# Performance work log

Measured on AMD Instinct MI355X. Metric: run time of the kernel, lower is better.

## Reference

```python
import jax, jax.numpy as jnp
import numpy as np

EMBED_DIM = 1024
NUM_HEADS = 16
HEAD_DIM = EMBED_DIM // NUM_HEADS
ROPE_BASE = 10000.0


def setup_inputs() -> dict:
    key = jax.random.key(0)
    ks = jax.random.split(key, 5)
    B, S, E = 4, 2048, EMBED_DIM
    hidden = jax.random.normal(ks[0], (B, S, E), dtype=jnp.float32)
    sc_in = 1.0 / np.sqrt(E)
    qkv_w = jax.random.normal(ks[1], (3 * E, E), dtype=jnp.float32) * sc_in
    qkv_b = jnp.zeros((3 * E,), dtype=jnp.float32)
    proj_w = jax.random.normal(ks[2], (E, E), dtype=jnp.float32) * sc_in
    proj_b = jnp.zeros((E,), dtype=jnp.float32)
    return {"hidden": hidden, "qkv_w": qkv_w, "qkv_b": qkv_b,
            "proj_w": proj_w, "proj_b": proj_b}


def _rope_cos_sin(position_ids, head_dim, base):
    # position_ids: [B, S] int; returns cos/sin of shape [B, 1, S, head_dim]
    inv_freq = 1.0 / (base ** (jnp.arange(0, head_dim, 2, dtype=jnp.float32) / head_dim))
    freqs = position_ids.astype(jnp.float32)[..., None] * inv_freq  # [B,S,hd/2]
    emb = jnp.concatenate([freqs, freqs], axis=-1)                  # [B,S,hd]
    return jnp.cos(emb)[:, None], jnp.sin(emb)[:, None]


def _rotate_half(x):
    x1, x2 = jnp.split(x, 2, axis=-1)
    return jnp.concatenate([-x2, x1], axis=-1)


def reference(hidden, qkv_w, qkv_b, proj_w, proj_b):
    B, S, E = hidden.shape
    H, hd = NUM_HEADS, HEAD_DIM
    qkv = hidden @ qkv_w.T + qkv_b                    # [B,S,3E]
    qkv = qkv.reshape(B, S, 3, H, hd).transpose(2, 0, 3, 1, 4)  # [3,B,H,S,hd]
    q, k, v = qkv[0], qkv[1], qkv[2]
    pos = jnp.broadcast_to(jnp.arange(S)[None, :], (B, S))
    cos, sin = _rope_cos_sin(pos, hd, ROPE_BASE)      # [B,1,S,hd]
    q = q * cos + _rotate_half(q) * sin
    k = k * cos + _rotate_half(k) * sin
    scale = 1.0 / jnp.sqrt(jnp.float32(hd))
    scores = jnp.einsum("bhsd,bhtd->bhst", q, k) * scale
    attn = jax.nn.softmax(scores, axis=-1)
    out = jnp.einsum("bhst,bhtd->bhsd", attn, v)      # [B,H,S,hd]
    out = out.transpose(0, 2, 1, 3).reshape(B, S, E)
    return out @ proj_w.T + proj_b
```

## Files before the change

kernel.cpp:

```cpp
#include <hip/hip_runtime.h>
#include <cstdint>
#include <cstddef>

typedef _Float16 f16;
typedef __attribute__((ext_vector_type(4))) float f32x4;
typedef __attribute__((ext_vector_type(8))) _Float16 f16x8;
typedef __attribute__((ext_vector_type(4))) _Float16 f16x4;

#define S_SEQ 2048
#define E_DIM 1024

#define OFF_HID   0ull
#define OFF_QKVW  8388608ull
#define OFF_PROJW 11534336ull
#define OFF_Q     12582912ull
#define OFF_K     20971520ull
#define OFF_VT    29360128ull
#define OFF_AO    37748736ull

__device__ __forceinline__ void async_copy16(const void* g, void* l) {
  __builtin_amdgcn_global_load_lds(
      (const __attribute__((address_space(1))) unsigned int*)g,
      (__attribute__((address_space(3))) unsigned int*)l, 16, 0, 0);
}

__device__ __forceinline__ f16x8 lds_read_b128(const f16* p) {
  f16x8 r;
  const __attribute__((address_space(3))) f16* p3 =
      (const __attribute__((address_space(3))) f16*)p;
  asm volatile("ds_read_b128 %0, %1" : "=v"(r) : "v"(p3));
  return r;
}

__device__ __forceinline__ float fast_exp2(float x) {
#if __has_builtin(__builtin_amdgcn_exp2f)
  return __builtin_amdgcn_exp2f(x);
#else
  return __expf(x * 0.6931471805599453f);
#endif
}

__device__ __forceinline__ int2 xcd_swizzle() {
  int lin = blockIdx.y * gridDim.x + blockIdx.x;
  int by = ((lin & 7) << 3) | ((lin >> 3) & 7);
  int bx = lin >> 6;
  return make_int2(bx, by);
}

__global__ __launch_bounds__(256) void cvt_kernel(const float* __restrict__ hid,
                                                  const float* __restrict__ qw,
                                                  const float* __restrict__ pw,
                                                  f16* __restrict__ ws) {
  long i = (long)blockIdx.x * 256 + threadIdx.x;
  const float* src;
  f16* dst;
  long idx;
  if (i < 2097152L) { src = hid; dst = ws + OFF_HID;  idx = i; }
  else if (i < 2883584L) { src = qw; dst = ws + OFF_QKVW; idx = i - 2097152L; }
  else { src = pw; dst = ws + OFF_PROJW; idx = i - 2883584L; }
  float4 v = *(const float4*)(src + idx * 4);
  f16x4 o = { (f16)v.x, (f16)v.y, (f16)v.z, (f16)v.w };
  *(f16x4*)(dst + idx * 4) = o;
}

template <int MODE>
__global__ __launch_bounds__(256)
void gemm_kernel(const f16* __restrict__ A, const f16* __restrict__ Bm,
                 const float* __restrict__ bias,
                 f16* __restrict__ q_out, f16* __restrict__ k_out,
                 f16* __restrict__ vT_out, float* __restrict__ f_out) {
  __shared__ __align__(16) f16 As[2][2][128 * 32];
  __shared__ __align__(16) f16 Bs[2][2][128 * 32];
  const int tid = threadIdx.x;
  const int wave = tid >> 6;
  const int lane = tid & 63;
  const int q4 = lane >> 4;
  const int l16 = lane & 15;
  const int2 sw = xcd_swizzle();
  const int bxs = sw.x;
  const int m0 = sw.y * 128;
  const int n0 = bxs * 128;
  const int wr = (wave >> 1) * 64;
  const int wc = (wave & 1) * 64;
  f32x4 acc[4][4] = {};

  const int srow = tid >> 2;
  const int scol = (tid & 3) * 8;

  auto stage = [&](int kt, int kh, int b) {
    const f16* as = A + (size_t)(m0 + srow) * 1024 + kt * 64 + kh * 32 + scol;
    async_copy16(as,             &As[b][kh][wave * 512]);
    async_copy16(as + 64 * 1024, &As[b][kh][2048 + wave * 512]);
    const f16* bs = Bm + (size_t)(n0 + srow) * 1024 + kt * 64 + kh * 32 + scol;
    async_copy16(bs,             &Bs[b][kh][wave * 512]);
    async_copy16(bs + 64 * 1024, &Bs[b][kh][2048 + wave * 512]);
  };

#define PHASE(T, KH, DO_STAGE, VMN)                                          \
  {                                                                          \
    const int cb_ = (T) & 1;                                                 \
    f16x8 af[4], bf[4];                                                      \
    _Pragma("unroll")                                                        \
    for (int mt = 0; mt < 4; ++mt)                                           \
      af[mt] = lds_read_b128(&As[cb_][KH][(wr + mt * 16 + l16) * 32 + q4 * 8]); \
    _Pragma("unroll")                                                        \
    for (int nt = 0; nt < 4; ++nt)                                           \
      bf[nt] = lds_read_b128(&Bs[cb_][KH][(wc + nt * 16 + l16) * 32 + q4 * 8]); \
    if (DO_STAGE) stage((T) + 1, KH, cb_ ^ 1);                               \
    __builtin_amdgcn_s_barrier();                                            \
    asm volatile("s_waitcnt lgkmcnt(0)" ::: "memory");                       \
    __builtin_amdgcn_sched_barrier(0);                                       \
    __builtin_amdgcn_s_setprio(1);                                           \
    _Pragma("unroll")                                                        \
    for (int mt = 0; mt < 4; ++mt)                                           \
      _Pragma("unroll")                                                      \
      for (int nt = 0; nt < 4; ++nt)                                         \
        acc[mt][nt] = __builtin_amdgcn_mfma_f32_16x16x32_f16(                \
            af[mt], bf[nt], acc[mt][nt], 0, 0, 0);                           \
    __builtin_amdgcn_s_setprio(0);                                           \
    __builtin_amdgcn_sched_barrier(0);                                       \
    asm volatile("s_waitcnt vmcnt(" #VMN ")" ::: "memory");                  \
    __builtin_amdgcn_s_barrier();                                            \
  }

  stage(0, 0, 0);
  stage(0, 1, 0);
  asm volatile("s_waitcnt vmcnt(4)" ::: "memory");
  __builtin_amdgcn_s_barrier();

  for (int t = 0; t < 15; ++t) {
    PHASE(t, 0, 1, 4);
    PHASE(t, 1, 1, 4);
  }
  PHASE(15, 0, 0, 0);
  PHASE(15, 1, 0, 0);
#undef PHASE

  if constexpr (MODE == 0) {
    const int part = bxs >> 3;
    const int h = (((bxs & 7) * 128) + wc) >> 6;
    float bv[4];
    for (int nt = 0; nt < 4; ++nt) bv[nt] = bias[n0 + wc + nt * 16 + l16];
    if (part < 2) {
      f16* outp = (part == 0) ? q_out : k_out;
      const float qscale = (part == 0) ? 0.18033688011112042f : 1.0f;
      float invf[2];
      for (int nt = 0; nt < 2; ++nt)
        invf[nt] = __expf(-(float)(nt * 16 + l16) * 0.2878231366242557f);
      for (int mt = 0; mt < 4; ++mt) {
        int mbase = m0 + wr + mt * 16 + q4 * 4;
        for (int r = 0; r < 4; ++r) {
          int mm = mbase + r;
          int b = mm >> 11, s = mm & 2047;
          size_t rowb = ((size_t)((b * 16 + h) * 2048 + s)) * 64;
          for (int nt = 0; nt < 2; ++nt) {
            float x1 = acc[mt][nt][r] + bv[nt];
            float x2 = acc[mt][nt + 2][r] + bv[nt + 2];
            float ang = (float)s * invf[nt];
            float sn, cs;
            __sincosf(ang, &sn, &cs);
            float o1 = (x1 * cs - x2 * sn) * qscale;
            float o2 = (x2 * cs + x1 * sn) * qscale;
            int d1 = nt * 16 + l16;
            outp[rowb + d1] = (f16)o1;
            outp[rowb + d1 + 32] = (f16)o2;
          }
        }
      }
    } else {
      for (int mt = 0; mt < 4; ++mt) {
        int mbase = m0 + wr + mt * 16 + q4 * 4;
        int b = mbase >> 11, s0 = mbase & 2047;
        for (int nt = 0; nt < 4; ++nt) {
          int d = nt * 16 + l16;
          size_t basei = ((size_t)((b * 16 + h) * 64 + d)) * 2048 + s0;
          f16x4 pk;
          for (int r = 0; r < 4; ++r) pk[r] = (f16)(acc[mt][nt][r] + bv[nt]);
          *(f16x4*)&vT_out[basei] = pk;
        }
      }
    }
  } else {
    float bv[4];
    for (int nt = 0; nt < 4; ++nt) bv[nt] = bias[n0 + wc + nt * 16 + l16];
    for (int mt = 0; mt < 4; ++mt)
      for (int r = 0; r < 4; ++r) {
        int mm = m0 + wr + mt * 16 + q4 * 4 + r;
        for (int nt = 0; nt < 4; ++nt)
          f_out[(size_t)mm * 1024 + n0 + wc + nt * 16 + l16] = acc[mt][nt][r] + bv[nt];
      }
  }
}

__global__ __launch_bounds__(256, 2)
void attn_kernel(const f16* __restrict__ Qg, const f16* __restrict__ Kg,
                 const f16* __restrict__ VTg, f16* __restrict__ AOg) {
  __shared__ __align__(16) f16 smem[2][8704];
  const int tid = threadIdx.x;
  const int wave = tid >> 6, lane = tid & 63;
  const int q4 = lane >> 4, l16 = lane & 15;
  const int2 sw = xcd_swizzle();
  const int qt = sw.x, bh = sw.y;
  const f16* Qb = Qg + (size_t)bh * (S_SEQ * 64);
  const f16* Kb = Kg + (size_t)bh * (S_SEQ * 64);
  const f16* Vb = VTg + (size_t)bh * (64 * S_SEQ);
  const int ws0 = wave * 64;

  f16x8 qf[4][2];
#pragma unroll
  for (int sn = 0; sn < 4; ++sn)
#pragma unroll
    for (int kf = 0; kf < 2; ++kf)
      qf[sn][kf] = *(const f16x8*)(Qb + (size_t)(qt * 256 + ws0 + sn * 16 + l16) * 64
                                      + kf * 32 + q4 * 8);

  f32x4 o[4][4] = {};
  f32x4 lacc[4] = {};
  f16x8 ones;
#pragma unroll
  for (int j = 0; j < 8; ++j) ones[j] = (f16)1.0f;

  const int srow = tid >> 3;
  const int scol = (tid & 7) * 8;

  const int kcs = scol >> 5;
  const int hs8 = ((scol >> 4) & 1) * 8;
  const int q0s = (scol & 15) >> 2;
  const int slot0 = kcs * 4 + q0s;
  const int swzA = (((slot0) ^ (srow & 7)) << 4) + hs8;
  const int swzB = (((slot0 + 1) ^ (srow & 7)) << 4) + hs8;

  int4 k0r = *(const int4*)(Kb + (size_t)srow * 64 + scol);
  int4 k1r = *(const int4*)(Kb + (size_t)(32 + srow) * 64 + scol);
  f16x8 v0r = *(const f16x8*)(Vb + (size_t)srow * 2048 + scol);
  f16x8 v1r = *(const f16x8*)(Vb + (size_t)(32 + srow) * 2048 + scol);
  {
    f16* Kn = smem[0];
    char* Vn = (char*)(smem[0] + 4608);
    *(int4*)(Kn + srow * 72 + scol) = k0r;
    *(int4*)(Kn + (32 + srow) * 72 + scol) = k1r;
    f16x4 lo0 = {v0r[0], v0r[1], v0r[2], v0r[3]};
    f16x4 hi0 = {v0r[4], v0r[5], v0r[6], v0r[7]};
    f16x4 lo1 = {v1r[0], v1r[1], v1r[2], v1r[3]};
    f16x4 hi1 = {v1r[4], v1r[5], v1r[6], v1r[7]};
    *(f16x4*)(Vn + srow * 128 + swzA) = lo0;
    *(f16x4*)(Vn + srow * 128 + swzB) = hi0;
    *(f16x4*)(Vn + (32 + srow) * 128 + swzA) = lo1;
    *(f16x4*)(Vn + (32 + srow) * 128 + swzB) = hi1;
  }
  __syncthreads();

  int cur = 0;
  for (int tt = 0; tt < 32; ++tt) {
    const f16* Kc = smem[cur];
    const char* Vc = (const char*)(smem[cur] + 4608);

    if (tt + 1 < 32) {
      const int t0n = (tt + 1) * 64;
      k0r = *(const int4*)(Kb + (size_t)(t0n + srow) * 64 + scol);
      k1r = *(const int4*)(Kb + (size_t)(t0n + 32 + srow) * 64 + scol);
      v0r = *(const f16x8*)(Vb + (size_t)srow * 2048 + t0n + scol);
      v1r = *(const f16x8*)(Vb + (size_t)(32 + srow) * 2048 + t0n + scol);
    }

    f16x8 kf0[4], kf1[4];
#pragma unroll
    for (int tm = 0; tm < 4; ++tm) {
      kf0[tm] = *(const f16x8*)(Kc + (tm * 16 + l16) * 72 + q4 * 8);
      kf1[tm] = *(const f16x8*)(Kc + (tm * 16 + l16) * 72 + 32 + q4 * 8);
    }
    f16x8 vf[4][2];
#pragma unroll
    for (int dm = 0; dm < 4; ++dm)
#pragma unroll
      for (int kc = 0; kc < 2; ++kc)
        vf[dm][kc] = *(const f16x8*)(Vc + (dm * 16 + l16) * 128 +
                                     (((kc * 4 + q4) ^ (l16 & 7)) << 4));

#pragma unroll
    for (int sn = 0; sn < 4; ++sn) {
      f32x4 st[4];
      __builtin_amdgcn_s_setprio(1);
#pragma unroll
      for (int tm = 0; tm < 4; ++tm) {
        f32x4 c = {0.f, 0.f, 0.f, 0.f};
        c = __builtin_amdgcn_mfma_f32_16x16x32_f16(kf0[tm], qf[sn][0], c, 0, 0, 0);
        c = __builtin_amdgcn_mfma_f32_16x16x32_f16(kf1[tm], qf[sn][1], c, 0, 0, 0);
        st[tm] = c;
      }
      __builtin_amdgcn_s_setprio(0);
#pragma unroll
      for (int tm = 0; tm < 4; ++tm)
#pragma unroll
        for (int r = 0; r < 4; ++r)
          st[tm][r] = fast_exp2(st[tm][r]);
#pragma unroll
      for (int kc = 0; kc < 2; ++kc) {
        f16x8 pf;
        pf[0] = (f16)st[kc * 2][0];
        pf[1] = (f16)st[kc * 2][1];
        pf[2] = (f16)st[kc * 2][2];
        pf[3] = (f16)st[kc * 2][3];
        pf[4] = (f16)st[kc * 2 + 1][0];
        pf[5] = (f16)st[kc * 2 + 1][1];
        pf[6] = (f16)st[kc * 2 + 1][2];
        pf[7] = (f16)st[kc * 2 + 1][3];
        __builtin_amdgcn_s_setprio(1);
        lacc[sn] = __builtin_amdgcn_mfma_f32_16x16x32_f16(ones, pf, lacc[sn], 0, 0, 0);
#pragma unroll
        for (int dm = 0; dm < 4; ++dm)
          o[dm][sn] = __builtin_amdgcn_mfma_f32_16x16x32_f16(vf[dm][kc], pf,
                                                             o[dm][sn], 0, 0, 0);
        __builtin_amdgcn_s_setprio(0);
      }
    }

    if (tt + 1 < 32) {
      f16* Kn = smem[cur ^ 1];
      char* Vn = (char*)(smem[cur ^ 1] + 4608);
      *(int4*)(Kn + srow * 72 + scol) = k0r;
      *(int4*)(Kn + (32 + srow) * 72 + scol) = k1r;
      f16x4 lo0 = {v0r[0], v0r[1], v0r[2], v0r[3]};
      f16x4 hi0 = {v0r[4], v0r[5], v0r[6], v0r[7]};
      f16x4 lo1 = {v1r[0], v1r[1], v1r[2], v1r[3]};
      f16x4 hi1 = {v1r[4], v1r[5], v1r[6], v1r[7]};
      *(f16x4*)(Vn + srow * 128 + swzA) = lo0;
      *(f16x4*)(Vn + srow * 128 + swzB) = hi0;
      *(f16x4*)(Vn + (32 + srow) * 128 + swzA) = lo1;
      *(f16x4*)(Vn + (32 + srow) * 128 + swzB) = hi1;
    }
    __syncthreads();
    cur ^= 1;
  }

  float inv_l[4];
#pragma unroll
  for (int sn = 0; sn < 4; ++sn) inv_l[sn] = 1.0f / lacc[sn][0];
  f16* Ot = smem[0];
#pragma unroll
  for (int sn = 0; sn < 4; ++sn) {
    int so = ws0 + sn * 16 + l16;
#pragma unroll
    for (int dm = 0; dm < 4; ++dm) {
      f16x4 w;
      w[0] = (f16)(o[dm][sn][0] * inv_l[sn]);
      w[1] = (f16)(o[dm][sn][1] * inv_l[sn]);
      w[2] = (f16)(o[dm][sn][2] * inv_l[sn]);
      w[3] = (f16)(o[dm][sn][3] * inv_l[sn]);
      *(f16x4*)(Ot + so * 64 + dm * 16 + q4 * 4) = w;
    }
  }
  __syncthreads();
  const int b = bh >> 4, h = bh & 15;
#pragma unroll
  for (int half = 0; half < 2; ++half) {
    const int sr = half * 128 + (tid >> 1), dh = (tid & 1) * 32;
    size_t gbase = ((size_t)(b * 2048 + qt * 256 + sr)) * 1024 + h * 64 + dh;
#pragma unroll
    for (int c = 0; c < 4; ++c) {
      f16x8 v = *(const f16x8*)(Ot + sr * 64 + dh + c * 8);
      *(f16x8*)(AOg + gbase + c * 8) = v;
    }
  }
}

extern "C" void kernel_launch(void* const* d_in, const int* in_sizes, int n_in,
                              void* d_out, int out_size, void* d_ws, size_t ws_size,
                              hipStream_t stream) {
  const float* hid   = (const float*)d_in[0];
  const float* qkvw  = (const float*)d_in[1];
  const float* qkvb  = (const float*)d_in[2];
  const float* projw = (const float*)d_in[3];
  const float* projb = (const float*)d_in[4];
  float* out = (float*)d_out;
  f16* ws = (f16*)d_ws;

  cvt_kernel<<<12288, 256, 0, stream>>>(hid, qkvw, projw, ws);
  gemm_kernel<0><<<dim3(24, 64), 256, 0, stream>>>(
      ws + OFF_HID, ws + OFF_QKVW, qkvb,
      ws + OFF_Q, ws + OFF_K, ws + OFF_VT, nullptr);
  attn_kernel<<<dim3(8, 64), 256, 0, stream>>>(
      ws + OFF_Q, ws + OFF_K, ws + OFF_VT, ws + OFF_AO);
  gemm_kernel<1><<<dim3(8, 64), 256, 0, stream>>>(
      ws + OFF_AO, ws + OFF_PROJW, projb,
      nullptr, nullptr, nullptr, out);
}
```

Measured before the change: 265.4 us.

## Load K and V fragments directly from global memory, dropping LDS staging

Removes the shared-memory double buffer for K and V tiles and has each wave load its MFMA fragments straight from global memory. K fragments are prefetched one tile ahead in registers, with two sets alternating. The setprio hints are dropped. This saves the LDS write/read traffic and the per-tile __syncthreads, but each of the four waves now fetches the same K/V data separately, relying on L1/L2 hits. V is read as 8-byte strided loads from the transposed layout, which are less coalesced.

New measurement: 362.0 us. 1.36x slower.

```diff
diff --git a/kernel.cpp b/kernel.cpp
--- a/kernel.cpp
+++ b/kernel.cpp
@@ -195,7 +195,7 @@
 __global__ __launch_bounds__(256, 2)
 void attn_kernel(const f16* __restrict__ Qg, const f16* __restrict__ Kg,
                  const f16* __restrict__ VTg, f16* __restrict__ AOg) {
-  __shared__ __align__(16) f16 smem[2][8704];
+  __shared__ __align__(16) f16 Ot[256 * 64];
   const int tid = threadIdx.x;
   const int wave = tid >> 6, lane = tid & 63;
   const int q4 = lane >> 4, l16 = lane & 15;
@@ -220,123 +220,88 @@
 #pragma unroll
   for (int j = 0; j < 8; ++j) ones[j] = (f16)1.0f;
 
-  const int srow = tid >> 3;
-  const int scol = (tid & 7) * 8;
-
-  const int kcs = scol >> 5;
-  const int hs8 = ((scol >> 4) & 1) * 8;
-  const int q0s = (scol & 15) >> 2;
-  const int slot0 = kcs * 4 + q0s;
-  const int swzA = (((slot0) ^ (srow & 7)) << 4) + hs8;
-  const int swzB = (((slot0 + 1) ^ (srow & 7)) << 4) + hs8;
-
-  int4 k0r = *(const int4*)(Kb + (size_t)srow * 64 + scol);
-  int4 k1r = *(const int4*)(Kb + (size_t)(32 + srow) * 64 + scol);
-  f16x8 v0r = *(const f16x8*)(Vb + (size_t)srow * 2048 + scol);
-  f16x8 v1r = *(const f16x8*)(Vb + (size_t)(32 + srow) * 2048 + scol);
-  {
-    f16* Kn = smem[0];
-    char* Vn = (char*)(smem[0] + 4608);
-    *(int4*)(Kn + srow * 72 + scol) = k0r;
-    *(int4*)(Kn + (32 + srow) * 72 + scol) = k1r;
-    f16x4 lo0 = {v0r[0], v0r[1], v0r[2], v0r[3]};
-    f16x4 hi0 = {v0r[4], v0r[5], v0r[6], v0r[7]};
-    f16x4 lo1 = {v1r[0], v1r[1], v1r[2], v1r[3]};
-    f16x4 hi1 = {v1r[4], v1r[5], v1r[6], v1r[7]};
-    *(f16x4*)(Vn + srow * 128 + swzA) = lo0;
-    *(f16x4*)(Vn + srow * 128 + swzB) = hi0;
-    *(f16x4*)(Vn + (32 + srow) * 128 + swzA) = lo1;
-    *(f16x4*)(Vn + (32 + srow) * 128 + swzB) = hi1;
-  }
-  __syncthreads();
-
-  int cur = 0;
-  for (int tt = 0; tt < 32; ++tt) {
-    const f16* Kc = smem[cur];
-    const char* Vc = (const char*)(smem[cur] + 4608);
-
-    if (tt + 1 < 32) {
-      const int t0n = (tt + 1) * 64;
-      k0r = *(const int4*)(Kb + (size_t)(t0n + srow) * 64 + scol);
-      k1r = *(const int4*)(Kb + (size_t)(t0n + 32 + srow) * 64 + scol);
-      v0r = *(const f16x8*)(Vb + (size_t)srow * 2048 + t0n + scol);
-      v1r = *(const f16x8*)(Vb + (size_t)(32 + srow) * 2048 + t0n + scol);
-    }
-
-    f16x8 kf0[4], kf1[4];
-#pragma unroll
-    for (int tm = 0; tm < 4; ++tm) {
-      kf0[tm] = *(const f16x8*)(Kc + (tm * 16 + l16) * 72 + q4 * 8);
-      kf1[tm] = *(const f16x8*)(Kc + (tm * 16 + l16) * 72 + 32 + q4 * 8);
-    }
-    f16x8 vf[4][2];
-#pragma unroll
-    for (int dm = 0; dm < 4; ++dm)
-#pragma unroll
-      for (int kc = 0; kc < 2; ++kc)
-        vf[dm][kc] = *(const f16x8*)(Vc + (dm * 16 + l16) * 128 +
-                                     (((kc * 4 + q4) ^ (l16 & 7)) << 4));
-
-#pragma unroll
-    for (int sn = 0; sn < 4; ++sn) {
-      f32x4 st[4];
-      __builtin_amdgcn_s_setprio(1);
-#pragma unroll
-      for (int tm = 0; tm < 4; ++tm) {
-        f32x4 c = {0.f, 0.f, 0.f, 0.f};
-        c = __builtin_amdgcn_mfma_f32_16x16x32_f16(kf0[tm], qf[sn][0], c, 0, 0, 0);
-        c = __builtin_amdgcn_mfma_f32_16x16x32_f16(kf1[tm], qf[sn][1], c, 0, 0, 0);
-        st[tm] = c;
-      }
-      __builtin_amdgcn_s_setprio(0);
-#pragma unroll
-      for (int tm = 0; tm < 4; ++tm)
-#pragma unroll
-        for (int r = 0; r < 4; ++r)
-          st[tm][r] = fast_exp2(st[tm][r]);
-#pragma unroll
-      for (int kc = 0; kc < 2; ++kc) {
-        f16x8 pf;
-        pf[0] = (f16)st[kc * 2][0];
-        pf[1] = (f16)st[kc * 2][1];
-        pf[2] = (f16)st[kc * 2][2];
-        pf[3] = (f16)st[kc * 2][3];
-        pf[4] = (f16)st[kc * 2 + 1][0];
-        pf[5] = (f16)st[kc * 2 + 1][1];
-        pf[6] = (f16)st[kc * 2 + 1][2];
-        pf[7] = (f16)st[kc * 2 + 1][3];
-        __builtin_amdgcn_s_setprio(1);
-        lacc[sn] = __builtin_amdgcn_mfma_f32_16x16x32_f16(ones, pf, lacc[sn], 0, 0, 0);
-#pragma unroll
-        for (int dm = 0; dm < 4; ++dm)
-          o[dm][sn] = __builtin_amdgcn_mfma_f32_16x16x32_f16(vf[dm][kc], pf,
-                                                             o[dm][sn], 0, 0, 0);
-        __builtin_amdgcn_s_setprio(0);
-      }
-    }
-
-    if (tt + 1 < 32) {
-      f16* Kn = smem[cur ^ 1];
-      char* Vn = (char*)(smem[cur ^ 1] + 4608);
-      *(int4*)(Kn + srow * 72 + scol) = k0r;
-      *(int4*)(Kn + (32 + srow) * 72 + scol) = k1r;
-      f16x4 lo0 = {v0r[0], v0r[1], v0r[2], v0r[3]};
-      f16x4 hi0 = {v0r[4], v0r[5], v0r[6], v0r[7]};
-      f16x4 lo1 = {v1r[0], v1r[1], v1r[2], v1r[3]};
-      f16x4 hi1 = {v1r[4], v1r[5], v1r[6], v1r[7]};
-      *(f16x4*)(Vn + srow * 128 + swzA) = lo0;
-      *(f16x4*)(Vn + srow * 128 + swzB) = hi0;
-      *(f16x4*)(Vn + (32 + srow) * 128 + swzA) = lo1;
-      *(f16x4*)(Vn + (32 + srow) * 128 + swzB) = hi1;
-    }
-    __syncthreads();
-    cur ^= 1;
-  }
+#define LOAD_K(TT, KF0, KF1)                                                 \
+  {                                                                          \
+    const f16* Kt_ = Kb + (size_t)(TT) * 4096;                               \
+    _Pragma("unroll")                                                        \
+    for (int tm = 0; tm < 4; ++tm) {                                         \
+      KF0[tm] = *(const f16x8*)(Kt_ + (tm * 16 + l16) * 64 + q4 * 8);        \
+      KF1[tm] = *(const f16x8*)(Kt_ + (tm * 16 + l16) * 64 + 32 + q4 * 8);   \
+    }                                                                        \
+  }
+
+#define LOAD_V(TT, VF)                                                       \
+  {                                                                          \
+    const f16* Vt_ = Vb + (size_t)(TT) * 64;                                 \
+    _Pragma("unroll")                                                        \
+    for (int dm = 0; dm < 4; ++dm)                                           \
+      _Pragma("unroll")                                                      \
+      for (int kc = 0; kc < 2; ++kc) {                                       \
+        const f16* vr_ = Vt_ + (size_t)(dm * 16 + l16) * 2048 + kc * 32 + q4 * 4; \
+        f16x4 lo_ = *(const f16x4*)vr_;                                      \
+        f16x4 hi_ = *(const f16x4*)(vr_ + 16);                               \
+        f16x8 v_;                                                            \
+        v_[0] = lo_[0]; v_[1] = lo_[1]; v_[2] = lo_[2]; v_[3] = lo_[3];      \
+        v_[4] = hi_[0]; v_[5] = hi_[1]; v_[6] = hi_[2]; v_[7] = hi_[3];      \
+        VF[dm][kc] = v_;                                                     \
+      }                                                                      \
+  }
+
+#define COMPUTE(KF0, KF1, VF)                                                \
+  {                                                                          \
+    _Pragma("unroll")                                                        \
+    for (int sn = 0; sn < 4; ++sn) {                                         \
+      f32x4 st[4];                                                           \
+      _Pragma("unroll")                                                      \
+      for (int tm = 0; tm < 4; ++tm) {                                       \
+        f32x4 c = {0.f, 0.f, 0.f, 0.f};                                      \
+        c = __builtin_amdgcn_mfma_f32_16x16x32_f16(KF0[tm], qf[sn][0], c, 0, 0, 0); \
+        c = __builtin_amdgcn_mfma_f32_16x16x32_f16(KF1[tm], qf[sn][1], c, 0, 0, 0); \
+        st[tm] = c;                                                          \
+      }                                                                      \
+      _Pragma("unroll")                                                      \
+      for (int tm = 0; tm < 4; ++tm)                                         \
+        _Pragma("unroll")                                                    \
+        for (int r = 0; r < 4; ++r)                                          \
+          st[tm][r] = fast_exp2(st[tm][r]);                                  \
+      _Pragma("unroll")                                                      \
+      for (int kc = 0; kc < 2; ++kc) {                                       \
+        f16x8 pf;                                                            \
+        pf[0] = (f16)st[kc * 2][0];                                          \
+        pf[1] = (f16)st[kc * 2][1];                                          \
+        pf[2] = (f16)st[kc * 2][2];                                          \
+        pf[3] = (f16)st[kc * 2][3];                                          \
+        pf[4] = (f16)st[kc * 2 + 1][0];                                      \
+        pf[5] = (f16)st[kc * 2 + 1][1];                                      \
+        pf[6] = (f16)st[kc * 2 + 1][2];                                      \
+        pf[7] = (f16)st[kc * 2 + 1][3];                                      \
+        lacc[sn] = __builtin_amdgcn_mfma_f32_16x16x32_f16(ones, pf, lacc[sn], 0, 0, 0); \
+        _Pragma("unroll")                                                    \
+        for (int dm = 0; dm < 4; ++dm)                                       \
+          o[dm][sn] = __builtin_amdgcn_mfma_f32_16x16x32_f16(VF[dm][kc], pf, \
+                                                             o[dm][sn], 0, 0, 0); \
+      }                                                                      \
+    }                                                                        \
+  }
+
+  f16x8 ka0[4], ka1[4], kb0[4], kb1[4];
+  f16x8 vv[4][2];
+  LOAD_K(0, ka0, ka1);
+  for (int tt = 0; tt < 32; tt += 2) {
+    LOAD_V(tt, vv);
+    LOAD_K(tt + 1, kb0, kb1);
+    COMPUTE(ka0, ka1, vv);
+    LOAD_V(tt + 1, vv);
+    if (tt + 2 < 32) LOAD_K(tt + 2, ka0, ka1);
+    COMPUTE(kb0, kb1, vv);
+  }
+#undef LOAD_K
+#undef LOAD_V
+#undef COMPUTE
 
   float inv_l[4];
 #pragma unroll
   for (int sn = 0; sn < 4; ++sn) inv_l[sn] = 1.0f / lacc[sn][0];
-  f16* Ot = smem[0];
 #pragma unroll
   for (int sn = 0; sn < 4; ++sn) {
     int so = ws0 + sn * 16 + l16;
```

## Halve attention query tile to raise occupancy and restructure inner MFMA loop

Applied to the files above, without the earlier changes.

The attention kernel now handles 128 query rows per block instead of 256, so each wave owns 32 rows, and the grid doubles to 1024 blocks. Launch bounds rise to 4 blocks per CU, with fewer per-wave accumulators and fragments to make room. The inner loop is reordered: K fragments are loaded per tile and reused across both query sub-tiles, V fragments are loaded per k-chunk, and the setprio hints are dropped. This trades more K/V reloads from global memory and LDS for more resident waves to hide exp and memory latency.

New measurement: 272.3 us. 1.03x slower.

```diff
diff --git a/kernel.cpp b/kernel.cpp
--- a/kernel.cpp
+++ b/kernel.cpp
@@ -192,7 +192,7 @@
   }
 }
 
-__global__ __launch_bounds__(256, 2)
+__global__ __launch_bounds__(256, 4)
 void attn_kernel(const f16* __restrict__ Qg, const f16* __restrict__ Kg,
                  const f16* __restrict__ VTg, f16* __restrict__ AOg) {
   __shared__ __align__(16) f16 smem[2][8704];
@@ -204,18 +204,18 @@
   const f16* Qb = Qg + (size_t)bh * (S_SEQ * 64);
   const f16* Kb = Kg + (size_t)bh * (S_SEQ * 64);
   const f16* Vb = VTg + (size_t)bh * (64 * S_SEQ);
-  const int ws0 = wave * 64;
-
-  f16x8 qf[4][2];
-#pragma unroll
-  for (int sn = 0; sn < 4; ++sn)
+  const int ws0 = wave * 32;
+
+  f16x8 qf[2][2];
+#pragma unroll
+  for (int sn = 0; sn < 2; ++sn)
 #pragma unroll
     for (int kf = 0; kf < 2; ++kf)
-      qf[sn][kf] = *(const f16x8*)(Qb + (size_t)(qt * 256 + ws0 + sn * 16 + l16) * 64
+      qf[sn][kf] = *(const f16x8*)(Qb + (size_t)(qt * 128 + ws0 + sn * 16 + l16) * 64
                                       + kf * 32 + q4 * 8);
 
-  f32x4 o[4][4] = {};
-  f32x4 lacc[4] = {};
+  f32x4 o[4][2] = {};
+  f32x4 lacc[2] = {};
   f16x8 ones;
 #pragma unroll
   for (int j = 0; j < 8; ++j) ones[j] = (f16)1.0f;
@@ -263,55 +263,58 @@
       v1r = *(const f16x8*)(Vb + (size_t)(32 + srow) * 2048 + t0n + scol);
     }
 
-    f16x8 kf0[4], kf1[4];
+    f32x4 st[2][4];
 #pragma unroll
     for (int tm = 0; tm < 4; ++tm) {
-      kf0[tm] = *(const f16x8*)(Kc + (tm * 16 + l16) * 72 + q4 * 8);
-      kf1[tm] = *(const f16x8*)(Kc + (tm * 16 + l16) * 72 + 32 + q4 * 8);
-    }
-    f16x8 vf[4][2];
-#pragma unroll
-    for (int dm = 0; dm < 4; ++dm)
-#pragma unroll
-      for (int kc = 0; kc < 2; ++kc)
-        vf[dm][kc] = *(const f16x8*)(Vc + (dm * 16 + l16) * 128 +
-                                     (((kc * 4 + q4) ^ (l16 & 7)) << 4));
-
-#pragma unroll
-    for (int sn = 0; sn < 4; ++sn) {
-      f32x4 st[4];
-      __builtin_amdgcn_s_setprio(1);
-#pragma unroll
-      for (int tm = 0; tm < 4; ++tm) {
+      f16x8 kf0 = *(const f16x8*)(Kc + (tm * 16 + l16) * 72 + q4 * 8);
+      f16x8 kf1 = *(const f16x8*)(Kc + (tm * 16 + l16) * 72 + 32 + q4 * 8);
+#pragma unroll
+      for (int sn = 0; sn < 2; ++sn) {
         f32x4 c = {0.f, 0.f, 0.f, 0.f};
-        c = __builtin_amdgcn_mfma_f32_16x16x32_f16(kf0[tm], qf[sn][0], c, 0, 0, 0);
-        c = __builtin_amdgcn_mfma_f32_16x16x32_f16(kf1[tm], qf[sn][1], c, 0, 0, 0);
-        st[tm] = c;
-      }
-      __builtin_amdgcn_s_setprio(0);
+        c = __builtin_amdgcn_mfma_f32_16x16x32_f16(kf0, qf[sn][0], c, 0, 0, 0);
+        c = __builtin_amdgcn_mfma_f32_16x16x32_f16(kf1, qf[sn][1], c, 0, 0, 0);
+        st[sn][tm] = c;
+      }
+    }
+
+    f16x8 pf[2][2];
+#pragma unroll
+    for (int sn = 0; sn < 2; ++sn) {
 #pragma unroll
       for (int tm = 0; tm < 4; ++tm)
 #pragma unroll
         for (int r = 0; r < 4; ++r)
-          st[tm][r] = fast_exp2(st[tm][r]);
+          st[sn][tm][r] = fast_exp2(st[sn][tm][r]);
 #pragma unroll
       for (int kc = 0; kc < 2; ++kc) {
-        f16x8 pf;
-        pf[0] = (f16)st[kc * 2][0];
-        pf[1] = (f16)st[kc * 2][1];
-        pf[2] = (f16)st[kc * 2][2];
-        pf[3] = (f16)st[kc * 2][3];
-        pf[4] = (f16)st[kc * 2 + 1][0];
-        pf[5] = (f16)st[kc * 2 + 1][1];
-        pf[6] = (f16)st[kc * 2 + 1][2];
-        pf[7] = (f16)st[kc * 2 + 1][3];
-        __builtin_amdgcn_s_setprio(1);
-        lacc[sn] = __builtin_amdgcn_mfma_f32_16x16x32_f16(ones, pf, lacc[sn], 0, 0, 0);
+        f16x8 p;
+        p[0] = (f16)st[sn][kc * 2][0];
+        p[1] = (f16)st[sn][kc * 2][1];
+        p[2] = (f16)st[sn][kc * 2][2];
+        p[3] = (f16)st[sn][kc * 2][3];
+        p[4] = (f16)st[sn][kc * 2 + 1][0];
+        p[5] = (f16)st[sn][kc * 2 + 1][1];
+        p[6] = (f16)st[sn][kc * 2 + 1][2];
+        p[7] = (f16)st[sn][kc * 2 + 1][3];
+        pf[sn][kc] = p;
+      }
+    }
+
+#pragma unroll
+    for (int kc = 0; kc < 2; ++kc) {
+      f16x8 vf[4];
+#pragma unroll
+      for (int dm = 0; dm < 4; ++dm)
+        vf[dm] = *(const f16x8*)(Vc + (dm * 16 + l16) * 128 +
+                                 (((kc * 4 + q4) ^ (l16 & 7)) << 4));
+#pragma unroll
+      for (int sn = 0; sn < 2; ++sn) {
+        lacc[sn] = __builtin_amdgcn_mfma_f32_16x16x32_f16(ones, pf[sn][kc],
+                                                          lacc[sn], 0, 0, 0);
 #pragma unroll
         for (int dm = 0; dm < 4; ++dm)
-          o[dm][sn] = __builtin_amdgcn_mfma_f32_16x16x32_f16(vf[dm][kc], pf,
+          o[dm][sn] = __builtin_amdgcn_mfma_f32_16x16x32_f16(vf[dm], pf[sn][kc],
                                                              o[dm][sn], 0, 0, 0);
-        __builtin_amdgcn_s_setprio(0);
       }
     }
 
@@ -333,12 +336,12 @@
     cur ^= 1;
   }
 
-  float inv_l[4];
-#pragma unroll
-  for (int sn = 0; sn < 4; ++sn) inv_l[sn] = 1.0f / lacc[sn][0];
+  float inv_l[2];
+#pragma unroll
+  for (int sn = 0; sn < 2; ++sn) inv_l[sn] = 1.0f / lacc[sn][0];
   f16* Ot = smem[0];
 #pragma unroll
-  for (int sn = 0; sn < 4; ++sn) {
+  for (int sn = 0; sn < 2; ++sn) {
     int so = ws0 + sn * 16 + l16;
 #pragma unroll
     for (int dm = 0; dm < 4; ++dm) {
@@ -352,15 +355,12 @@
   }
   __syncthreads();
   const int b = bh >> 4, h = bh & 15;
-#pragma unroll
-  for (int half = 0; half < 2; ++half) {
-    const int sr = half * 128 + (tid >> 1), dh = (tid & 1) * 32;
-    size_t gbase = ((size_t)(b * 2048 + qt * 256 + sr)) * 1024 + h * 64 + dh;
-#pragma unroll
-    for (int c = 0; c < 4; ++c) {
-      f16x8 v = *(const f16x8*)(Ot + sr * 64 + dh + c * 8);
-      *(f16x8*)(AOg + gbase + c * 8) = v;
-    }
+  const int sr = tid >> 1, dh = (tid & 1) * 32;
+  size_t gbase = ((size_t)(b * 2048 + qt * 128 + sr)) * 1024 + h * 64 + dh;
+#pragma unroll
+  for (int c = 0; c < 4; ++c) {
+    f16x8 v = *(const f16x8*)(Ot + sr * 64 + dh + c * 8);
+    *(f16x8*)(AOg + gbase + c * 8) = v;
   }
 }
 
@@ -379,7 +379,7 @@
   gemm_kernel<0><<<dim3(24, 64), 256, 0, stream>>>(
       ws + OFF_HID, ws + OFF_QKVW, qkvb,
       ws + OFF_Q, ws + OFF_K, ws + OFF_VT, nullptr);
-  attn_kernel<<<dim3(8, 64), 256, 0, stream>>>(
+  attn_kernel<<<dim3(16, 64), 256, 0, stream>>>(
       ws + OFF_Q, ws + OFF_K, ws + OFF_VT, ws + OFF_AO);
   gemm_kernel<1><<<dim3(8, 64), 256, 0, stream>>>(
       ws + OFF_AO, ws + OFF_PROJW, projb,
```
